# Optimization experiments

Hardware: AMD Instinct MI355X
Metric: run time of the kernel (lower is better)

The kernel has to match this reference:

```python
import jax, jax.numpy as jnp
import numpy as np

N_WIRES = 8


def setup_inputs() -> dict:
    key = jax.random.key(0)
    k1, k2, k3 = jax.random.split(key, 3)
    B, S, E = 8, 1024, 64
    x = jax.random.normal(k1, (B, S, E), jnp.float32)
    theta = jax.random.normal(k2, (N_WIRES,), jnp.float32) * 0.1  # trainable RX angles (shared QLayer across heads)
    V_CAT = 16
    combine_w = jax.random.normal(k3, (E, V_CAT), jnp.float32) / jnp.sqrt(jnp.float32(V_CAT))
    combine_b = jnp.zeros((E,), jnp.float32)
    return {"x": x, "theta": theta, "combine_w": combine_w, "combine_b": combine_b}


def _cnot(state, c, t):
    # state: [N] + [2]*N_WIRES ; wire w lives on axis w+1
    ca, ta = c + 1, t + 1
    s0 = jax.lax.index_in_dim(state, 0, axis=ca, keepdims=False)
    s1 = jax.lax.index_in_dim(state, 1, axis=ca, keepdims=False)
    ta2 = ta - 1 if ta > ca else ta  # control axis was removed
    s1 = jnp.flip(s1, axis=ta2)      # flip target bit where control == 1
    return jnp.stack([s0, s1], axis=ca)


def _qlayer(angles, theta):
    # angles: [N, 8]. RX(x) then trainable RX(theta) on same wire == RX(x+theta).
    half = 0.5 * (angles + theta)
    amp0 = jnp.cos(half).astype(jnp.complex64)          # <0|RX|0>
    amp1 = (-1j) * jnp.sin(half).astype(jnp.complex64)  # <1|RX|0>
    N = angles.shape[0]
    # product state over 8 wires -> [N, 256]
    state = jnp.ones((N, 1), jnp.complex64)
    for w in range(N_WIRES):
        per = jnp.stack([amp0[:, w], amp1[:, w]], axis=-1)  # [N, 2]
        state = (state[:, :, None] * per[:, None, :]).reshape(N, -1)
    state = state.reshape((N,) + (2,) * N_WIRES)
    # CNOT chain 0->1, ..., 6->7, then ring closure 7->0
    for w in range(N_WIRES - 1):
        state = _cnot(state, w, w + 1)
    state = _cnot(state, N_WIRES - 1, 0)
    probs = state.real ** 2 + state.imag ** 2
    exps = []
    for w in range(N_WIRES):
        axes = tuple(ax for ax in range(1, N_WIRES + 1) if ax != w + 1)
        marg = probs.sum(axis=axes)  # [N, 2]
        exps.append(marg[:, 0] - marg[:, 1])  # <Z_w>
    return jnp.stack(exps, axis=-1)  # [N, 8]


def reference(x, theta, combine_w, combine_b):
    B, S, E = x.shape
    d_k = E // N_WIRES  # == 8 (encoder needs exactly 8 angles)
    heads = x.reshape(B, S, N_WIRES, d_k).transpose(0, 2, 1, 3)  # [B, H, S, 8]
    meas = _qlayer(heads.reshape(-1, d_k), theta).reshape(B, N_WIRES, S, N_WIRES)
    # torch.chunk(3, -1) on size 8 -> splits of 3, 3, 2
    q, k, v = meas[..., :3], meas[..., 3:6], meas[..., 6:]
    scores = jnp.einsum('bhsd,bhtd->bhst', q, k) / jnp.sqrt(jnp.float32(E))
    attn = jax.nn.softmax(scores, axis=-1)
    out = jnp.einsum('bhst,bhtd->bhsd', attn, v)          # [B, H, S, 2]
    out = out.transpose(0, 2, 1, 3).reshape(B, S, -1)     # [B, S, 16]
    return out @ combine_w.T + combine_b
```

## Files before the change

### kernel.cpp

```cpp
#include <hip/hip_runtime.h>
#include <hip/hip_fp16.h>

#define NB 8
#define NS 1024
#define NH 8
#define NMONO 56
#define MPART 512


constexpr int PRED[NMONO] = {
    0,
    0, 0, 0,
    1, 2, 3, 2, 3, 3,
    4, 5, 6, 7, 8, 9, 7, 8, 9, 9,
    10,11,12,13,14,15,16,17,18,19,16,17,18,19,19,
    20,21,22,23,24,25,26,27,28,29,30,31,32,33,34,30,31,32,33,34,34};
constexpr int VARI[NMONO] = {
    0,
    0, 1, 2,
    0, 0, 0, 1, 1, 2,
    0, 0, 0, 0, 0, 0, 1, 1, 1, 2,
    0, 0, 0, 0, 0, 0, 0, 0, 0, 0, 1, 1, 1, 1, 2,
    0, 0, 0, 0, 0, 0, 0, 0, 0, 0, 0, 0, 0, 0, 0, 1, 1, 1, 1, 1, 2};
#define F6 0.166666666666667f
#define F12 0.0833333333333333f
#define F24 0.0416666666666667f
#define F120 0.00833333333333333f
constexpr float COEF[NMONO] = {
    1.f,
    1.f, 1.f, 1.f,
    0.5f, 1.f, 1.f, 0.5f, 1.f, 0.5f,
    F6, 0.5f, 0.5f, 0.5f, 1.f, 0.5f, F6, 0.5f, 0.5f, F6,
    F24, F6, F6, 0.25f, 0.5f, 0.25f, F6, 0.5f, 0.5f, F6, F24, F6, 0.25f, F6, F24,
    F120, F24, F24, F12, F6, F12, F12, 0.25f, 0.25f, F12, F24, F6, 0.25f, F6, F24,
    F120, F24, F12, F12, F24, F120};

__global__ __launch_bounds__(192) void moments_kernel(
        const float* __restrict__ x, const float* __restrict__ theta,
        float* __restrict__ part) {
    __shared__ float red[3][64][57];

    const int tid = threadIdx.x;
    const int bh = blockIdx.x >> 3;
    const int qt = blockIdx.x & 7;
    const int b = bh >> 3, h = bh & 7;
    const int t0 = qt * 128;

    float th[8];
#pragma unroll
    for (int j = 0; j < 8; ++j) th[j] = theta[j];

    const int w = tid >> 6, l = tid & 63;

    float acc[NMONO];
#pragma unroll
    for (int i = 0; i < NMONO; ++i) acc[i] = 0.f;

#pragma unroll 1
    for (int j = 0; j < 2; ++j) {
        int t = t0 + l + 64 * j;
        const float4* xp = (const float4*)(x + ((size_t)(b * NS + t)) * 64 + h * 8);
        float4 lo = xp[0], hi = xp[1];
        float c0 = __cosf(lo.x + th[0]);
        float c1 = __cosf(lo.y + th[1]);
        float c2 = __cosf(lo.z + th[2]);
        float c3 = __cosf(lo.w + th[3]);
        float c4 = __cosf(hi.x + th[4]);
        float c5 = __cosf(hi.y + th[5]);
        float c6 = __cosf(hi.z + th[6]);
        float c7 = __cosf(hi.w + th[7]);
        float k0 = ((c0 * c1) * c2) * c3;
        float k1 = k0 * c4;
        float k2 = k1 * c5;
        float v0 = k2 * c6;
        float v1 = v0 * c7;
        float wch = (w == 0) ? 1.f : ((w == 1) ? v0 : v1);

        float mono[NMONO];
        mono[0] = wch;
        acc[0] += wch;
#pragma unroll
        for (int i = 1; i < NMONO; ++i) {
            float var = (VARI[i] == 0) ? k0 : ((VARI[i] == 1) ? k1 : k2);
            mono[i] = mono[PRED[i]] * var;
            acc[i] += mono[i];
        }
    }
#pragma unroll
    for (int i = 0; i < NMONO; ++i) red[w][l][i] = acc[i];
    __syncthreads();

    if (l < NMONO) {
        float s0 = 0.f, s1 = 0.f, s2 = 0.f, s3 = 0.f;
#pragma unroll
        for (int r = 0; r < 16; ++r) {
            s0 += red[w][4 * r + 0][l];
            s1 += red[w][4 * r + 1][l];
            s2 += red[w][4 * r + 2][l];
            s3 += red[w][4 * r + 3][l];
        }
        part[(size_t)blockIdx.x * 168 + w * 56 + l] = ((s0 + s1) + (s2 + s3)) * COEF[l];
    }
}

__global__ __launch_bounds__(256) void eval_proj_kernel(
        const float* __restrict__ x, const float* __restrict__ theta,
        const float* __restrict__ part, const float* __restrict__ W,
        const float* __restrict__ bias, float* __restrict__ out) {
    __shared__ __align__(16) float MhL[8 * 172];
    __shared__ float WtL[16 * 65];
    __shared__ float biasL[64];
    __shared__ float attL[16][17];

    const int tid = threadIdx.x;
    const int b = blockIdx.x >> 6;
    const int sc = blockIdx.x & 63;
    const int s0 = sc * 16;

    for (int e = tid; e < 8 * 168; e += 256) {
        int h = e / 168, idx = e - h * 168;
        const float* p = part + ((size_t)((b * 8 + h) * 8)) * 168 + idx;
        float s = ((p[0] + p[168]) + (p[336] + p[504]))
                + ((p[672] + p[840]) + (p[1008] + p[1176]));
        MhL[h * 172 + idx] = s;
    }
    for (int i = tid; i < 1024; i += 256) WtL[(i & 15) * 65 + (i >> 4)] = W[i];
    if (tid < 64) biasL[tid] = bias[tid];
    __syncthreads();

    if (tid < 128) {
        const int h = tid >> 4, sl = tid & 15;
        const int s = s0 + sl;
        float th[8];
#pragma unroll
        for (int j = 0; j < 8; ++j) th[j] = theta[j];
        const float4* xp = (const float4*)(x + ((size_t)(b * NS + s)) * 64 + h * 8);
        float4 lo = xp[0], hi = xp[1];
        float c0 = __cosf(lo.x + th[0]);
        float c1 = __cosf(lo.y + th[1]);
        float c2 = __cosf(lo.z + th[2]);
        float c3 = __cosf(lo.w + th[3]);
        float c4 = __cosf(hi.x + th[4]);
        float c5 = __cosf(hi.y + th[5]);
        float c6 = __cosf(hi.z + th[6]);
        float c7 = __cosf(hi.w + th[7]);
        float m1 = c0 * c1;
        float m2 = m1 * c2;
        float m0 = ((c1 * c2) * (c3 * c4)) * ((c5 * c6) * c7);
        float q0 = m0 * 0.125f, q1 = m1 * 0.125f, q2 = m2 * 0.125f;

        float mono[NMONO];
        mono[0] = 1.f;
#pragma unroll
        for (int i = 1; i < NMONO; ++i)
            mono[i] = mono[PRED[i]] * ((VARI[i] == 0) ? q0 : ((VARI[i] == 1) ? q1 : q2));

        const float4* MS = (const float4*)&MhL[h * 172];
        const float4* MA = (const float4*)&MhL[h * 172 + 56];
        const float4* MB = (const float4*)&MhL[h * 172 + 112];
        float aS = 0.f, aA = 0.f, aB = 0.f;
#pragma unroll
        for (int g = 0; g < 14; ++g) {
            float4 ms = MS[g], ma = MA[g], mb = MB[g];
            float p0 = mono[g * 4 + 0], p1 = mono[g * 4 + 1];
            float p2 = mono[g * 4 + 2], p3 = mono[g * 4 + 3];
            aS = fmaf(p0, ms.x, aS); aS = fmaf(p1, ms.y, aS);
            aS = fmaf(p2, ms.z, aS); aS = fmaf(p3, ms.w, aS);
            aA = fmaf(p0, ma.x, aA); aA = fmaf(p1, ma.y, aA);
            aA = fmaf(p2, ma.z, aA); aA = fmaf(p3, ma.w, aA);
            aB = fmaf(p0, mb.x, aB); aB = fmaf(p1, mb.y, aB);
            aB = fmaf(p2, mb.z, aB); aB = fmaf(p3, mb.w, aB);
        }
        float inv = 1.0f / aS;
        attL[sl][2 * h]     = aA * inv;
        attL[sl][2 * h + 1] = aB * inv;
    }
    __syncthreads();

    {
        const int e = tid & 63, rr = tid >> 6;
#pragma unroll
        for (int j = 0; j < 4; ++j) {
            int row = rr * 4 + j;
            float acc = biasL[e];
#pragma unroll
            for (int jj = 0; jj < 16; ++jj)
                acc = fmaf(attL[row][jj], WtL[jj * 65 + e], acc);
            out[((size_t)(b * NS + s0 + row)) * 64 + e] = acc;
        }
    }
}

#define NPAD 1028
#define SPB 32
__global__ __launch_bounds__(256) void fused_kernel(const float* __restrict__ x,
                                                    const float* __restrict__ theta,
                                                    const float* __restrict__ W,
                                                    const float* __restrict__ bias,
                                                    float* __restrict__ out) {
    __shared__ __half2 kvA[NH][NPAD];
    __shared__ __half2 kvB[NH][NPAD];
    __shared__ __half  kvC[NH][NPAD];
    __shared__ float   attl[SPB][17];
    __shared__ float   Wt[16][64];
    __shared__ float   bl[64];

    const int tid = threadIdx.x;
    const int b = blockIdx.x >> 5;
    const int chunk = blockIdx.x & 31;

    float th[8];
#pragma unroll
    for (int j = 0; j < 8; ++j) th[j] = theta[j];

    for (int i = tid; i < 1024; i += 256) Wt[i & 15][i >> 4] = W[i];
    if (tid < 64) bl[tid] = bias[tid];

    for (int i = 0; i < 32; ++i) {
        int r = tid + (i << 8);
        int h = r & 7, t = r >> 3;
        const float4* xp = (const float4*)(x + (((size_t)(b * NS + t)) << 6) + h * 8);
        float4 lo = xp[0], hi = xp[1];
        float c0 = __cosf(lo.x + th[0]);
        float c1 = __cosf(lo.y + th[1]);
        float c2 = __cosf(lo.z + th[2]);
        float c3 = __cosf(lo.w + th[3]);
        float c4 = __cosf(hi.x + th[4]);
        float c5 = __cosf(hi.y + th[5]);
        float c6 = __cosf(hi.z + th[6]);
        float c7 = __cosf(hi.w + th[7]);
        float m3 = ((c0 * c1) * c2) * c3;
        float m4 = m3 * c4;
        float m5 = m4 * c5;
        float m6 = m5 * c6;
        float m7 = m6 * c7;
        kvA[h][t] = __floats2half2_rn(m3, m4);
        kvB[h][t] = __floats2half2_rn(m5, m6);
        kvC[h][t] = __float2half_rn(m7);
    }
    __syncthreads();

    {
        const int h = tid >> 5;
        const int sl = tid & 31;
        const int sg = chunk * SPB + sl;
        const float4* xp = (const float4*)(x + (((size_t)(b * NS + sg)) << 6) + h * 8);
        float4 lo = xp[0], hi = xp[1];
        float c0 = __cosf(lo.x + th[0]);
        float c1 = __cosf(lo.y + th[1]);
        float c2 = __cosf(lo.z + th[2]);
        float c3 = __cosf(lo.w + th[3]);
        float c4 = __cosf(hi.x + th[4]);
        float c5 = __cosf(hi.y + th[5]);
        float c6 = __cosf(hi.z + th[6]);
        float c7 = __cosf(hi.w + th[7]);
        float m1 = c0 * c1;
        float m2 = m1 * c2;
        float m0 = ((c1 * c2) * (c3 * c4)) * ((c5 * c6) * c7);
        float q0 = m0 * 0.125f, q1 = m1 * 0.125f, q2 = m2 * 0.125f;

        float sum = 0.f, a0 = 0.f, a1 = 0.f;
#pragma unroll 4
        for (int t = 0; t < NS; ++t) {
            float2 kk = __half22float2(kvA[h][t]);
            float2 kv = __half22float2(kvB[h][t]);
            float v1 = __half2float(kvC[h][t]);
            float sc = q0 * kk.x + q1 * kk.y + q2 * kv.x;
            float e = __expf(sc);
            sum += e;
            a0 += e * kv.y;
            a1 += e * v1;
        }
        float inv = 1.0f / sum;
        attl[sl][h * 2] = a0 * inv;
        attl[sl][h * 2 + 1] = a1 * inv;
    }
    __syncthreads();

    {
        const int e = tid & 63;
        const int rr = tid >> 6;
#pragma unroll
        for (int i = 0; i < 8; ++i) {
            int sl = rr * 8 + i;
            float acc = bl[e];
#pragma unroll
            for (int j = 0; j < 16; ++j)
                acc += attl[sl][j] * Wt[j][e];
            int sg = chunk * SPB + sl;
            out[(((size_t)(b * NS + sg)) << 6) + e] = acc;
        }
    }
}

extern "C" void kernel_launch(void* const* d_in, const int* in_sizes, int n_in,
                              void* d_out, int out_size, void* d_ws, size_t ws_size,
                              hipStream_t stream) {
    const float* x     = (const float*)d_in[0];
    const float* theta = (const float*)d_in[1];
    const float* W     = (const float*)d_in[2];
    const float* bias  = (const float*)d_in[3];
    float* out = (float*)d_out;

    if (ws_size >= (size_t)MPART * 168 * sizeof(float)) {
        float* part = (float*)d_ws;
        moments_kernel<<<dim3(MPART), dim3(192), 0, stream>>>(x, theta, part);
        eval_proj_kernel<<<dim3(512), dim3(256), 0, stream>>>(x, theta, part, W, bias, out);
    } else {
        fused_kernel<<<dim3(NB * (NS / SPB)), dim3(256), 0, stream>>>(x, theta, W, bias, out);
    }
}
```

Before: 69.86 us.

## Fuse moment accumulation and evaluation into a single kernel with redundant per-block moments

Replaces the two-kernel scheme (moment partial sums to workspace, then evaluation and projection) with one kernel. Each block recomputes the full 1024-key Taylor moments for all 8 heads of its batch, reduces them with warp shuffles and shared memory, then evaluates 32 query rows and the output projection. This removes a launch and the global round-trip of partial sums, but every block now repeats the moment computation, giving 32x redundant work per batch and heavy register pressure from three 56-element accumulators.

```diff
diff --git a/kernel.cpp b/kernel.cpp
--- a/kernel.cpp
+++ b/kernel.cpp
@@ -1,11 +1,9 @@
 #include <hip/hip_runtime.h>
-#include <hip/hip_fp16.h>
 
 #define NB 8
 #define NS 1024
 #define NH 8
 #define NMONO 56
-#define MPART 512
 
 
 constexpr int PRED[NMONO] = {
@@ -35,30 +33,38 @@
     F120, F24, F24, F12, F6, F12, F12, 0.25f, 0.25f, F12, F24, F6, 0.25f, F6, F24,
     F120, F24, F12, F12, F24, F120};
 
-__global__ __launch_bounds__(192) void moments_kernel(
+__global__ __launch_bounds__(512, 2) void fused_qattn_kernel(
         const float* __restrict__ x, const float* __restrict__ theta,
-        float* __restrict__ part) {
-    __shared__ float red[3][64][57];
+        const float* __restrict__ W, const float* __restrict__ bias,
+        float* __restrict__ out) {
+    __shared__ __align__(16) float redL[8][8][168];
+    __shared__ __align__(16) float MhL[8 * 172];
+    __shared__ float WtL[16 * 65];
+    __shared__ float biasL[64];
+    __shared__ float attL[32][17];
 
     const int tid = threadIdx.x;
-    const int bh = blockIdx.x >> 3;
-    const int qt = blockIdx.x & 7;
-    const int b = bh >> 3, h = bh & 7;
-    const int t0 = qt * 128;
+    const int b = blockIdx.x >> 5;
+    const int chunk = blockIdx.x & 31;
+    const int s0 = chunk * 32;
 
     float th[8];
 #pragma unroll
     for (int j = 0; j < 8; ++j) th[j] = theta[j];
 
-    const int w = tid >> 6, l = tid & 63;
-
-    float acc[NMONO];
-#pragma unroll
-    for (int i = 0; i < NMONO; ++i) acc[i] = 0.f;
+    for (int i = tid; i < 1024; i += 512) WtL[(i & 15) * 65 + (i >> 4)] = W[i];
+    if (tid < 64) biasL[tid] = bias[tid];
+
+    const int h = tid & 7;
+    const int tslot = tid >> 3;
+
+    float accS[NMONO], accA[NMONO], accB[NMONO];
+#pragma unroll
+    for (int i = 0; i < NMONO; ++i) { accS[i] = 0.f; accA[i] = 0.f; accB[i] = 0.f; }
 
 #pragma unroll 1
-    for (int j = 0; j < 2; ++j) {
-        int t = t0 + l + 64 * j;
+    for (int it = 0; it < 16; ++it) {
+        const int t = tslot + 64 * it;
         const float4* xp = (const float4*)(x + ((size_t)(b * NS + t)) * 64 + h * 8);
         float4 lo = xp[0], hi = xp[1];
         float c0 = __cosf(lo.x + th[0]);
@@ -74,67 +80,64 @@
         float k2 = k1 * c5;
         float v0 = k2 * c6;
         float v1 = v0 * c7;
-        float wch = (w == 0) ? 1.f : ((w == 1) ? v0 : v1);
 
         float mono[NMONO];
-        mono[0] = wch;
-        acc[0] += wch;
+        mono[0] = 1.f;
+        accS[0] += 1.f;
+        accA[0] += v0;
+        accB[0] += v1;
 #pragma unroll
         for (int i = 1; i < NMONO; ++i) {
             float var = (VARI[i] == 0) ? k0 : ((VARI[i] == 1) ? k1 : k2);
             mono[i] = mono[PRED[i]] * var;
-            acc[i] += mono[i];
+            accS[i] += mono[i];
+            accA[i] = fmaf(mono[i], v0, accA[i]);
+            accB[i] = fmaf(mono[i], v1, accB[i]);
         }
     }
-#pragma unroll
-    for (int i = 0; i < NMONO; ++i) red[w][l][i] = acc[i];
+
+#pragma unroll
+    for (int i = 0; i < NMONO; ++i) {
+        float a = accS[i];
+        a += __shfl_xor(a, 8); a += __shfl_xor(a, 16); a += __shfl_xor(a, 32);
+        accS[i] = a;
+        float p = accA[i];
+        p += __shfl_xor(p, 8); p += __shfl_xor(p, 16); p += __shfl_xor(p, 32);
+        accA[i] = p;
+        float q = accB[i];
+        q += __shfl_xor(q, 8); q += __shfl_xor(q, 16); q += __shfl_xor(q, 32);
+        accB[i] = q;
+    }
+
+    const int wv = tid >> 6;
+    const int l  = tid & 63;
+    if (l < 8) {
+        float* dst = &redL[wv][l][0];
+#pragma unroll
+        for (int g = 0; g < 14; ++g)
+            ((float4*)dst)[g] = make_float4(accS[4*g], accS[4*g+1], accS[4*g+2], accS[4*g+3]);
+#pragma unroll
+        for (int g = 0; g < 14; ++g)
+            ((float4*)(dst + 56))[g] = make_float4(accA[4*g], accA[4*g+1], accA[4*g+2], accA[4*g+3]);
+#pragma unroll
+        for (int g = 0; g < 14; ++g)
+            ((float4*)(dst + 112))[g] = make_float4(accB[4*g], accB[4*g+1], accB[4*g+2], accB[4*g+3]);
+    }
     __syncthreads();
 
-    if (l < NMONO) {
-        float s0 = 0.f, s1 = 0.f, s2 = 0.f, s3 = 0.f;
-#pragma unroll
-        for (int r = 0; r < 16; ++r) {
-            s0 += red[w][4 * r + 0][l];
-            s1 += red[w][4 * r + 1][l];
-            s2 += red[w][4 * r + 2][l];
-            s3 += red[w][4 * r + 3][l];
-        }
-        part[(size_t)blockIdx.x * 168 + w * 56 + l] = ((s0 + s1) + (s2 + s3)) * COEF[l];
-    }
-}
-
-__global__ __launch_bounds__(256) void eval_proj_kernel(
-        const float* __restrict__ x, const float* __restrict__ theta,
-        const float* __restrict__ part, const float* __restrict__ W,
-        const float* __restrict__ bias, float* __restrict__ out) {
-    __shared__ __align__(16) float MhL[8 * 172];
-    __shared__ float WtL[16 * 65];
-    __shared__ float biasL[64];
-    __shared__ float attL[16][17];
-
-    const int tid = threadIdx.x;
-    const int b = blockIdx.x >> 6;
-    const int sc = blockIdx.x & 63;
-    const int s0 = sc * 16;
-
-    for (int e = tid; e < 8 * 168; e += 256) {
-        int h = e / 168, idx = e - h * 168;
-        const float* p = part + ((size_t)((b * 8 + h) * 8)) * 168 + idx;
-        float s = ((p[0] + p[168]) + (p[336] + p[504]))
-                + ((p[672] + p[840]) + (p[1008] + p[1176]));
-        MhL[h * 172 + idx] = s;
-    }
-    for (int i = tid; i < 1024; i += 256) WtL[(i & 15) * 65 + (i >> 4)] = W[i];
-    if (tid < 64) biasL[tid] = bias[tid];
+    for (int e = tid; e < 8 * 168; e += 512) {
+        const int hh = e / 168, j = e - hh * 168;
+        float s = 0.f;
+#pragma unroll
+        for (int ww = 0; ww < 8; ++ww) s += redL[ww][hh][j];
+        MhL[hh * 172 + j] = s * COEF[j % 56];
+    }
     __syncthreads();
 
-    if (tid < 128) {
-        const int h = tid >> 4, sl = tid & 15;
+    if (tid < 256) {
+        const int eh = tid >> 5, sl = tid & 31;
         const int s = s0 + sl;
-        float th[8];
-#pragma unroll
-        for (int j = 0; j < 8; ++j) th[j] = theta[j];
-        const float4* xp = (const float4*)(x + ((size_t)(b * NS + s)) * 64 + h * 8);
+        const float4* xp = (const float4*)(x + ((size_t)(b * NS + s)) * 64 + eh * 8);
         float4 lo = xp[0], hi = xp[1];
         float c0 = __cosf(lo.x + th[0]);
         float c1 = __cosf(lo.y + th[1]);
@@ -155,9 +158,9 @@
         for (int i = 1; i < NMONO; ++i)
             mono[i] = mono[PRED[i]] * ((VARI[i] == 0) ? q0 : ((VARI[i] == 1) ? q1 : q2));
 
-        const float4* MS = (const float4*)&MhL[h * 172];
-        const float4* MA = (const float4*)&MhL[h * 172 + 56];
-        const float4* MB = (const float4*)&MhL[h * 172 + 112];
+        const float4* MS = (const float4*)&MhL[eh * 172];
+        const float4* MA = (const float4*)&MhL[eh * 172 + 56];
+        const float4* MB = (const float4*)&MhL[eh * 172 + 112];
         float aS = 0.f, aA = 0.f, aB = 0.f;
 #pragma unroll
         for (int g = 0; g < 14; ++g) {
@@ -172,123 +175,21 @@
             aB = fmaf(p2, mb.z, aB); aB = fmaf(p3, mb.w, aB);
         }
         float inv = 1.0f / aS;
-        attL[sl][2 * h]     = aA * inv;
-        attL[sl][2 * h + 1] = aB * inv;
+        attL[sl][2 * eh]     = aA * inv;
+        attL[sl][2 * eh + 1] = aB * inv;
     }
     __syncthreads();
 
     {
-        const int e = tid & 63, rr = tid >> 6;
+        const int e = tid & 63, r0 = tid >> 6;
 #pragma unroll
         for (int j = 0; j < 4; ++j) {
-            int row = rr * 4 + j;
+            const int row = r0 + 8 * j;
             float acc = biasL[e];
 #pragma unroll
             for (int jj = 0; jj < 16; ++jj)
                 acc = fmaf(attL[row][jj], WtL[jj * 65 + e], acc);
             out[((size_t)(b * NS + s0 + row)) * 64 + e] = acc;
-        }
-    }
-}
-
-#define NPAD 1028
-#define SPB 32
-__global__ __launch_bounds__(256) void fused_kernel(const float* __restrict__ x,
-                                                    const float* __restrict__ theta,
-                                                    const float* __restrict__ W,
-                                                    const float* __restrict__ bias,
-                                                    float* __restrict__ out) {
-    __shared__ __half2 kvA[NH][NPAD];
-    __shared__ __half2 kvB[NH][NPAD];
-    __shared__ __half  kvC[NH][NPAD];
-    __shared__ float   attl[SPB][17];
-    __shared__ float   Wt[16][64];
-    __shared__ float   bl[64];
-
-    const int tid = threadIdx.x;
-    const int b = blockIdx.x >> 5;
-    const int chunk = blockIdx.x & 31;
-
-    float th[8];
-#pragma unroll
-    for (int j = 0; j < 8; ++j) th[j] = theta[j];
-
-    for (int i = tid; i < 1024; i += 256) Wt[i & 15][i >> 4] = W[i];
-    if (tid < 64) bl[tid] = bias[tid];
-
-    for (int i = 0; i < 32; ++i) {
-        int r = tid + (i << 8);
-        int h = r & 7, t = r >> 3;
-        const float4* xp = (const float4*)(x + (((size_t)(b * NS + t)) << 6) + h * 8);
-        float4 lo = xp[0], hi = xp[1];
-        float c0 = __cosf(lo.x + th[0]);
-        float c1 = __cosf(lo.y + th[1]);
-        float c2 = __cosf(lo.z + th[2]);
-        float c3 = __cosf(lo.w + th[3]);
-        float c4 = __cosf(hi.x + th[4]);
-        float c5 = __cosf(hi.y + th[5]);
-        float c6 = __cosf(hi.z + th[6]);
-        float c7 = __cosf(hi.w + th[7]);
-        float m3 = ((c0 * c1) * c2) * c3;
-        float m4 = m3 * c4;
-        float m5 = m4 * c5;
-        float m6 = m5 * c6;
-        float m7 = m6 * c7;
-        kvA[h][t] = __floats2half2_rn(m3, m4);
-        kvB[h][t] = __floats2half2_rn(m5, m6);
-        kvC[h][t] = __float2half_rn(m7);
-    }
-    __syncthreads();
-
-    {
-        const int h = tid >> 5;
-        const int sl = tid & 31;
-        const int sg = chunk * SPB + sl;
-        const float4* xp = (const float4*)(x + (((size_t)(b * NS + sg)) << 6) + h * 8);
-        float4 lo = xp[0], hi = xp[1];
-        float c0 = __cosf(lo.x + th[0]);
-        float c1 = __cosf(lo.y + th[1]);
-        float c2 = __cosf(lo.z + th[2]);
-        float c3 = __cosf(lo.w + th[3]);
-        float c4 = __cosf(hi.x + th[4]);
-        float c5 = __cosf(hi.y + th[5]);
-        float c6 = __cosf(hi.z + th[6]);
-        float c7 = __cosf(hi.w + th[7]);
-        float m1 = c0 * c1;
-        float m2 = m1 * c2;
-        float m0 = ((c1 * c2) * (c3 * c4)) * ((c5 * c6) * c7);
-        float q0 = m0 * 0.125f, q1 = m1 * 0.125f, q2 = m2 * 0.125f;
-
-        float sum = 0.f, a0 = 0.f, a1 = 0.f;
-#pragma unroll 4
-        for (int t = 0; t < NS; ++t) {
-            float2 kk = __half22float2(kvA[h][t]);
-            float2 kv = __half22float2(kvB[h][t]);
-            float v1 = __half2float(kvC[h][t]);
-            float sc = q0 * kk.x + q1 * kk.y + q2 * kv.x;
-            float e = __expf(sc);
-            sum += e;
-            a0 += e * kv.y;
-            a1 += e * v1;
-        }
-        float inv = 1.0f / sum;
-        attl[sl][h * 2] = a0 * inv;
-        attl[sl][h * 2 + 1] = a1 * inv;
-    }
-    __syncthreads();
-
-    {
-        const int e = tid & 63;
-        const int rr = tid >> 6;
-#pragma unroll
-        for (int i = 0; i < 8; ++i) {
-            int sl = rr * 8 + i;
-            float acc = bl[e];
-#pragma unroll
-            for (int j = 0; j < 16; ++j)
-                acc += attl[sl][j] * Wt[j][e];
-            int sg = chunk * SPB + sl;
-            out[(((size_t)(b * NS + sg)) << 6) + e] = acc;
         }
     }
 }
@@ -302,11 +203,5 @@
     const float* bias  = (const float*)d_in[3];
     float* out = (float*)d_out;
 
-    if (ws_size >= (size_t)MPART * 168 * sizeof(float)) {
-        float* part = (float*)d_ws;
-        moments_kernel<<<dim3(MPART), dim3(192), 0, stream>>>(x, theta, part);
-        eval_proj_kernel<<<dim3(512), dim3(256), 0, stream>>>(x, theta, part, W, bias, out);
-    } else {
-        fused_kernel<<<dim3(NB * (NS / SPB)), dim3(256), 0, stream>>>(x, theta, W, bias, out);
-    }
+    fused_qattn_kernel<<<dim3(NB * 32), dim3(512), 0, stream>>>(x, theta, W, bias, out);
 }
```

New measurement: 100.5 us. +43.9%, slower.
